# Kernel tuning notes

Measured on AMD Instinct MI355X. Metric: run time of the kernel, lower is better.

## Reference

```python
import jax, jax.numpy as jnp
import numpy as np

N = 4096      # batch (e.g. nodes)
MUL = 128     # multiplicity of every irrep chunk
INV_SQRT3 = 1.0 / float(np.sqrt(3.0))  # CG norm for 1x1->0 and 0x1->1 / 1x0->1
INV_SQRT6 = 1.0 / float(np.sqrt(6.0))  # CG norm for 1x1->1 (Levi-Civita / sqrt(6))

# Levi-Civita tensor eps[i,j,k]
_EPS = np.zeros((3, 3, 3), dtype=np.float32)
for a, b, c in [(0, 1, 2), (1, 2, 0), (2, 0, 1)]:
    _EPS[a, b, c] = 1.0
    _EPS[a, c, b] = -1.0
EPS = jnp.asarray(_EPS)


def setup_inputs() -> dict:
    key = jax.random.key(0)
    ks = jax.random.split(key, 9)
    # e3nn path normalization folded into weight init std:
    # std = 1/sqrt(mul1*mul2*num_paths_into_that_output_irrep)
    std2 = 1.0 / float(np.sqrt(MUL * MUL * 2))  # scalar out: 2 paths
    std3 = 1.0 / float(np.sqrt(MUL * MUL * 3))  # vector out: 3 paths
    W = (MUL, MUL, MUL)
    return {
        "x1_s": jax.random.normal(ks[0], (N, MUL), dtype=jnp.float32),
        "x1_v": jax.random.normal(ks[1], (N, MUL, 3), dtype=jnp.float32),
        "x2_s": jax.random.normal(ks[2], (N, MUL), dtype=jnp.float32),
        "x2_v": jax.random.normal(ks[3], (N, MUL, 3), dtype=jnp.float32),
        "w_sss": jax.random.normal(ks[4], W, dtype=jnp.float32) * std2,
        "w_vvs": jax.random.normal(ks[5], W, dtype=jnp.float32) * std2,
        "w_svv": jax.random.normal(ks[6], W, dtype=jnp.float32) * std3,
        "w_vsv": jax.random.normal(ks[7], W, dtype=jnp.float32) * std3,
        "w_vvv": jax.random.normal(ks[8], W, dtype=jnp.float32) * std3,
    }


def reference(x1_s, x1_v, x2_s, x2_v, w_sss, w_vvs, w_svv, w_vsv, w_vvv):
    # ---- paths into 0e (scalar) output ----
    # 0e x 0e -> 0e : CG = 1
    a = jnp.einsum('nu,uvw->nvw', x1_s, w_sss)           # [N,MUL,MUL]
    out_s = jnp.einsum('nvw,nv->nw', a, x2_s)            # [N,MUL]
    # 1o x 1o -> 0e : CG = delta_ij / sqrt(3)
    dot = jnp.einsum('nui,nvi->nuv', x1_v, x2_v) * INV_SQRT3
    out_s = out_s + jnp.einsum('nuv,uvw->nw', dot, w_vvs)
    # ---- paths into 1o (vector) output ----
    # 0e x 1o -> 1o : CG = delta / sqrt(3)
    b = jnp.einsum('nu,uvw->nvw', x1_s, w_svv)
    out_v = jnp.einsum('nvw,nvk->nwk', b, x2_v) * INV_SQRT3   # [N,MUL,3]
    # 1o x 0e -> 1o : CG = delta / sqrt(3)
    c = jnp.einsum('nv,uvw->nuw', x2_s, w_vsv)
    out_v = out_v + jnp.einsum('nuw,nuk->nwk', c, x1_v) * INV_SQRT3
    # 1o x 1o -> 1o : CG = eps_ijk / sqrt(6)  (cross product)
    c1 = jnp.einsum('nvj,ijk->nvik', x2_v, EPS)               # [N,MUL,3,3]
    cross = jnp.einsum('nui,nvik->nuvk', x1_v, c1)            # [N,MUL,MUL,3]
    out_v = out_v + jnp.einsum('nuvk,uvw->nwk', cross, w_vvv) * INV_SQRT6
    # pack IrrepsArray 128x0e+128x1o as flat [N, 128 + 384]
    return jnp.concatenate([out_s, out_v.reshape(out_v.shape[0], -1)], axis=-1)
```

## Files before the change

kernel.cpp:

```cpp
#include <hip/hip_runtime.h>
#include <hip/hip_bf16.h>


typedef _Float16 f16;
typedef _Float16 f16x8 __attribute__((ext_vector_type(8)));
typedef _Float16 h2 __attribute__((ext_vector_type(2)));
typedef float f32x4 __attribute__((ext_vector_type(4)));
typedef unsigned u32;

#define WT_BYTES  (5u*4u*128u*4096u*2u)
#define X1_BYTES  (64u*4u*8192u*2u)
#define SLICE_EL  1310720u
#define CHUNK_EL  10240u

__device__ __forceinline__ h2 bc(u32 x){ union{u32 u; h2 h;} c; c.u=x; return c.h; }

union F8 { h2 h[4]; f16x8 v; };

__device__ __forceinline__ void gl_lds16(const f16* g, f16* l) {
    __builtin_amdgcn_global_load_lds(
        (const __attribute__((address_space(1))) void*)g,
        (__attribute__((address_space(3))) void*)l,
        16, 0, 0);
}

__global__ __launch_bounds__(256) void pack_w_kernel(
    const float* __restrict__ w0, const float* __restrict__ w1,
    const float* __restrict__ w2, const float* __restrict__ w3,
    const float* __restrict__ w4, f16* __restrict__ wt)
{
    __shared__ float tl[64][130];
    const int b = blockIdx.x;
    const int p = b >> 7;
    const int u = b & 127;
    const int usec = u >> 5;
    const int uin  = u & 31;
    const float* src = (p==0)?w0:(p==1)?w1:(p==2)?w2:(p==3)?w3:w4;
    const float scale = (p==0)?1.0f:(p==4)?0.40824829046386302f:0.57735026918962576f;

    for (int h = 0; h < 2; ++h) {
        const float* spR = src + (size_t)u*16384 + (size_t)h*8192;
        #pragma unroll
        for (int k = 0; k < 8; ++k) {
            const int e4 = (k*256 + threadIdx.x) * 4;
            const float4 v4 = *(const float4*)(spR + e4);
            const int vi = e4 >> 7, w = e4 & 127;
            tl[vi][w+0]=v4.x; tl[vi][w+1]=v4.y; tl[vi][w+2]=v4.z; tl[vi][w+3]=v4.w;
        }
        __syncthreads();
        #pragma unroll
        for (int k = 0; k < 4; ++k) {
            const int cid = k*256 + threadIdx.x;
            const int q     = cid & 3;
            const int wg    = (cid >> 2) & 127;
            const int vbh   = cid >> 9;
            const int vb    = h*2 + vbh;
            const int c     = vb*32 + uin;
            const int whalf = wg >> 6;
            const int wl    = wg & 63;
            const int qs    = q ^ ((wl >> 1) & 3);
            f16x8 t8;
            #pragma unroll
            for (int j = 0; j < 8; ++j)
                t8[j] = (f16)(tl[vbh*32 + q*8 + j][wg] * scale);
            *(f16x8*)(wt + (size_t)(usec*2 + whalf)*SLICE_EL + (size_t)c*CHUNK_EL
                          + p*2048 + wl*32 + qs*8) = t8;
        }
        __syncthreads();
    }
}

__global__ __launch_bounds__(256) void pack_x_kernel(
    const float* __restrict__ x1s, const float* __restrict__ x1v,
    const float* __restrict__ x2s, const float* __restrict__ x2v,
    f16* __restrict__ x1g, f16* __restrict__ x2g)
{
    if (blockIdx.x < 128) {
        __shared__ uint2 tl[128][33];
        const int nb = blockIdx.x;
        #pragma unroll
        for (int k = 0; k < 16; ++k) {
            const int idx = k*256 + threadIdx.x;
            const int u = idx & 127, nd = idx >> 7;
            const size_t i = (size_t)(nb*32 + nd)*128 + u;
            union { f16 h[4]; uint2 u2; } tp;
            tp.h[0] = (f16)x1s[i];
            tp.h[1] = (f16)x1v[i*3 + 0];
            tp.h[2] = (f16)x1v[i*3 + 1];
            tp.h[3] = (f16)x1v[i*3 + 2];
            tl[u][nd] = tp.u2;
        }
        __syncthreads();
        uint2* og = (uint2*)x1g;
        const int t = nb >> 1, nd0 = (nb & 1) * 32;
        #pragma unroll
        for (int k = 0; k < 16; ++k) {
            const int idx = k*256 + threadIdx.x;
            const int u = idx >> 5, nd = idx & 31;
            og[(((t*4 + (u>>5))*32 + (u&31)) << 6) + nd0 + nd] = tl[u][nd];
        }
    } else {
        const int tt = (blockIdx.x - 128)*256 + threadIdx.x;
        const int n = tt >> 7, v = tt & 127;
        const size_t b = (size_t)n*512;
        const size_t i = (size_t)n*128 + v;
        x2g[b +   0 + v] = (f16)x2s[i];
        x2g[b + 128 + v] = (f16)x2v[i*3 + 0];
        x2g[b + 256 + v] = (f16)x2v[i*3 + 1];
        x2g[b + 384 + v] = (f16)x2v[i*3 + 2];
    }
}

__global__ __launch_bounds__(256, 2) void tp_main(
    const f16* __restrict__ wt, const f16* __restrict__ x1g,
    const f16* __restrict__ x2g, float* __restrict__ out)
{
    __shared__ __align__(16) f16 wlds[3*CHUNK_EL];
    __shared__ __align__(16) f16 x1lds[8192];

    const int tid  = threadIdx.x;
    const int lane = tid & 63;
    const int wv   = tid >> 6;
    const int kg   = lane >> 4;
    const int lr   = lane & 15;

    const int b     = blockIdx.x;
    const int slice = b & 7;
    const int t     = b >> 3;
    const int usec  = slice >> 1;
    const int whalf = slice & 1;

    const f16* wstream = wt + (size_t)slice * SLICE_EL;

    int boff[4];
    #pragma unroll
    for (int ct = 0; ct < 4; ++ct) {
        const int wp = ct*16 + lr;
        boff[ct] = wp*32 + ((kg ^ ((wp >> 1) & 3)) * 8);
    }

    {
        const f16* src = x1g + ((size_t)(t*4 + usec) << 13);
        #pragma unroll
        for (int r = 0; r < 4; ++r)
            gl_lds16(src + r*2048 + wv*512 + lane*8, x1lds + r*2048 + wv*512 + lane*8);
    }
    #pragma unroll
    for (int k = 0; k < 2; ++k)
        #pragma unroll
        for (int r = 0; r < 5; ++r)
            gl_lds16(wstream + k*CHUNK_EL + r*2048 + tid*8,
                     wlds    + k*CHUNK_EL + r*2048 + tid*8);
    __syncthreads();

    f32x4 acc[4][4];
    #pragma unroll
    for (int c2 = 0; c2 < 4; ++c2)
        #pragma unroll
        for (int d = 0; d < 4; ++d)
            acc[c2][d] = (f32x4){0.f, 0.f, 0.f, 0.f};

    h2 xq[4][4];
    const f16* wsrc = wstream + 2*CHUNK_EL + tid*8;
    const f16* x2base = x2g + ((size_t)(t*64 + wv*16 + lr) << 9) + kg*8;
    const int nodel4 = (wv*16 + lr) * 4;

    auto body = [&](int c, int bi) __attribute__((always_inline)) {
        if ((c & 31) == 0) {
            const f16* xb = x2base + (c >> 5)*32;
            const uint4 h0 = *(const uint4*)(xb);
            const uint4 h1 = *(const uint4*)(xb + 128);
            const uint4 h2v = *(const uint4*)(xb + 256);
            const uint4 h3 = *(const uint4*)(xb + 384);
            xq[0][0]=bc(h0.x); xq[0][1]=bc(h0.y); xq[0][2]=bc(h0.z); xq[0][3]=bc(h0.w);
            xq[1][0]=bc(h1.x); xq[1][1]=bc(h1.y); xq[1][2]=bc(h1.z); xq[1][3]=bc(h1.w);
            xq[2][0]=bc(h2v.x); xq[2][1]=bc(h2v.y); xq[2][2]=bc(h2v.z); xq[2][3]=bc(h2v.w);
            xq[3][0]=bc(h3.x); xq[3][1]=bc(h3.y); xq[3][2]=bc(h3.z); xq[3][3]=bc(h3.w);
        }

        if (c < 127) { asm volatile("s_waitcnt vmcnt(5)" ::: "memory"); }
        else         { asm volatile("s_waitcnt vmcnt(0)" ::: "memory"); }
        __builtin_amdgcn_s_barrier();
        __builtin_amdgcn_sched_barrier(0);

        if (c < 126) {
            f16* dc = wlds + ((bi + 2) % 3)*CHUNK_EL + tid*8;
            #pragma unroll
            for (int r = 0; r < 5; ++r)
                gl_lds16(wsrc + r*2048, dc + r*2048);
        }
        wsrc += CHUNK_EL;

        const int u2 = c & 31;

        const uint2 h1 = *(const uint2*)(x1lds + u2*256 + nodel4);
        const h2 ps1 = bc(__builtin_amdgcn_perm(h1.x, h1.x, 0x01000100u));
        h2 pv[3];
        pv[0] = bc(__builtin_amdgcn_perm(h1.x, h1.x, 0x03020302u));
        pv[1] = bc(__builtin_amdgcn_perm(h1.y, h1.y, 0x01000100u));
        pv[2] = bc(__builtin_amdgcn_perm(h1.y, h1.y, 0x03020302u));

        F8 f0, f1, fa[3], fb[3], fc[3];
        #pragma unroll
        for (int j = 0; j < 4; ++j) {
            f0.h[j] = ps1 * xq[0][j];
            h2 d = pv[0] * xq[1][j];
            d = __builtin_elementwise_fma(pv[1], xq[2][j], d);
            f1.h[j] = __builtin_elementwise_fma(pv[2], xq[3][j], d);
        }
        #pragma unroll
        for (int k = 0; k < 3; ++k) {
            const int k1 = (k+1) % 3, k2 = (k+2) % 3;
            #pragma unroll
            for (int j = 0; j < 4; ++j) {
                fa[k].h[j] = ps1   * xq[1+k][j];
                fb[k].h[j] = pv[k] * xq[0][j];
                h2 tx = pv[k1] * xq[1+k2][j];
                fc[k].h[j] = __builtin_elementwise_fma(-pv[k2], xq[1+k1][j], tx);
            }
        }

        const f16* wb = wlds + bi*CHUNK_EL;
        __builtin_amdgcn_s_setprio(1);
        #pragma unroll
        for (int ct = 0; ct < 4; ++ct) {
            const f16x8 b0 = *(const f16x8*)(wb +    0 + boff[ct]);
            const f16x8 b1 = *(const f16x8*)(wb + 2048 + boff[ct]);
            const f16x8 b2 = *(const f16x8*)(wb + 4096 + boff[ct]);
            const f16x8 b3 = *(const f16x8*)(wb + 6144 + boff[ct]);
            const f16x8 b4 = *(const f16x8*)(wb + 8192 + boff[ct]);
            acc[ct][0] = __builtin_amdgcn_mfma_f32_16x16x32_f16(f0.v, b0, acc[ct][0], 0,0,0);
            acc[ct][0] = __builtin_amdgcn_mfma_f32_16x16x32_f16(f1.v, b1, acc[ct][0], 0,0,0);
            #pragma unroll
            for (int k = 0; k < 3; ++k) {
                acc[ct][1+k] = __builtin_amdgcn_mfma_f32_16x16x32_f16(fa[k].v, b2, acc[ct][1+k], 0,0,0);
                acc[ct][1+k] = __builtin_amdgcn_mfma_f32_16x16x32_f16(fb[k].v, b3, acc[ct][1+k], 0,0,0);
                acc[ct][1+k] = __builtin_amdgcn_mfma_f32_16x16x32_f16(fc[k].v, b4, acc[ct][1+k], 0,0,0);
            }
        }
        __builtin_amdgcn_s_setprio(0);
    };

    for (int cb = 0; cb < 126; cb += 3) {
        body(cb + 0, 0);
        body(cb + 1, 1);
        body(cb + 2, 2);
    }
    body(126, 0);
    body(127, 1);

    #pragma unroll
    for (int ct = 0; ct < 4; ++ct) {
        const int w = whalf*64 + ct*16 + lr;
        #pragma unroll
        for (int j = 0; j < 4; ++j) {
            const int n = t*64 + wv*16 + kg*4 + j;
            float* op = out + (size_t)n*512;
            unsafeAtomicAdd(op + w,             acc[ct][0][j]);
            unsafeAtomicAdd(op + 128 + w*3 + 0, acc[ct][1][j]);
            unsafeAtomicAdd(op + 128 + w*3 + 1, acc[ct][2][j]);
            unsafeAtomicAdd(op + 128 + w*3 + 2, acc[ct][3][j]);
        }
    }
}

extern "C" void kernel_launch(void* const* d_in, const int* in_sizes, int n_in,
                              void* d_out, int out_size, void* d_ws, size_t ws_size,
                              hipStream_t stream)
{
    const float* x1s = (const float*)d_in[0];
    const float* x1v = (const float*)d_in[1];
    const float* x2s = (const float*)d_in[2];
    const float* x2v = (const float*)d_in[3];
    const float* w0  = (const float*)d_in[4];
    const float* w1  = (const float*)d_in[5];
    const float* w2  = (const float*)d_in[6];
    const float* w3  = (const float*)d_in[7];
    const float* w4  = (const float*)d_in[8];

    f16* wtb = (f16*)d_ws;
    f16* x1g = (f16*)((char*)d_ws + WT_BYTES);
    f16* x2g = (f16*)((char*)d_ws + WT_BYTES + X1_BYTES);
    float* out = (float*)d_out;

    pack_w_kernel<<<640, 256, 0, stream>>>(w0, w1, w2, w3, w4, wtb);
    pack_x_kernel<<<2176, 256, 0, stream>>>(x1s, x1v, x2s, x2v, x1g, x2g);
    hipMemsetAsync(d_out, 0, (size_t)out_size*sizeof(float), stream);
    tp_main<<<512, 256, 0, stream>>>(wtb, x1g, x2g, out);
}
```

Baseline: 240.2 us.

## Split v-range into halves for 1024 blocks, double-buffer weights, drop x1 LDS staging

Splits each block's reduction over v into two halves, so 16 slices per node tile and twice as many blocks. The weight packing is relaid to match. LDS shrinks from triple to double buffering and x1 is read straight from global with a one-step prefetch instead of staged in LDS, so occupancy can rise to 4 blocks per CU. The cost is twice as many atomic adds on the output, a full vmcnt(0) wait each step where the old code kept loads in flight, and the removal of setprio.

```diff
diff --git a/kernel.cpp b/kernel.cpp
--- a/kernel.cpp
+++ b/kernel.cpp
@@ -10,7 +10,7 @@
 
 #define WT_BYTES  (5u*4u*128u*4096u*2u)
 #define X1_BYTES  (64u*4u*8192u*2u)
-#define SLICE_EL  1310720u
+#define SLICE_EL  655360u
 #define CHUNK_EL  10240u
 
 __device__ __forceinline__ h2 bc(u32 x){ union{u32 u; h2 h;} c; c.u=x; return c.h; }
@@ -55,15 +55,17 @@
             const int wg    = (cid >> 2) & 127;
             const int vbh   = cid >> 9;
             const int vb    = h*2 + vbh;
-            const int c     = vb*32 + uin;
+            const int vhalf = vb >> 1;
+            const int c     = (vb & 1)*32 + uin;
             const int whalf = wg >> 6;
             const int wl    = wg & 63;
             const int qs    = q ^ ((wl >> 1) & 3);
+            const int s     = usec*4 + whalf*2 + vhalf;
             f16x8 t8;
             #pragma unroll
             for (int j = 0; j < 8; ++j)
                 t8[j] = (f16)(tl[vbh*32 + q*8 + j][wg] * scale);
-            *(f16x8*)(wt + (size_t)(usec*2 + whalf)*SLICE_EL + (size_t)c*CHUNK_EL
+            *(f16x8*)(wt + (size_t)s*SLICE_EL + (size_t)c*CHUNK_EL
                           + p*2048 + wl*32 + qs*8) = t8;
         }
         __syncthreads();
@@ -111,12 +113,11 @@
     }
 }
 
-__global__ __launch_bounds__(256, 2) void tp_main(
+__global__ __launch_bounds__(256, 4) void tp_main(
     const f16* __restrict__ wt, const f16* __restrict__ x1g,
     const f16* __restrict__ x2g, float* __restrict__ out)
 {
-    __shared__ __align__(16) f16 wlds[3*CHUNK_EL];
-    __shared__ __align__(16) f16 x1lds[8192];
+    __shared__ __align__(16) f16 wlds[2*CHUNK_EL];
 
     const int tid  = threadIdx.x;
     const int lane = tid & 63;
@@ -125,12 +126,13 @@
     const int lr   = lane & 15;
 
     const int b     = blockIdx.x;
-    const int slice = b & 7;
-    const int t     = b >> 3;
-    const int usec  = slice >> 1;
-    const int whalf = slice & 1;
-
-    const f16* wstream = wt + (size_t)slice * SLICE_EL;
+    const int s     = b & 15;
+    const int t     = b >> 4;
+    const int usec  = s >> 2;
+    const int whalf = (s >> 1) & 1;
+    const int vhalf = s & 1;
+
+    const f16* wstream = wt + (size_t)s * SLICE_EL;
 
     int boff[4];
     #pragma unroll
@@ -139,18 +141,14 @@
         boff[ct] = wp*32 + ((kg ^ ((wp >> 1) & 3)) * 8);
     }
 
-    {
-        const f16* src = x1g + ((size_t)(t*4 + usec) << 13);
-        #pragma unroll
-        for (int r = 0; r < 4; ++r)
-            gl_lds16(src + r*2048 + wv*512 + lane*8, x1lds + r*2048 + wv*512 + lane*8);
-    }
-    #pragma unroll
-    for (int k = 0; k < 2; ++k)
-        #pragma unroll
-        for (int r = 0; r < 5; ++r)
-            gl_lds16(wstream + k*CHUNK_EL + r*2048 + tid*8,
-                     wlds    + k*CHUNK_EL + r*2048 + tid*8);
+    const int nodel4 = (wv*16 + lr) * 4;
+    const f16* x1base = x1g + (size_t)(t*4 + usec) * 8192 + nodel4;
+    const f16* x2base = x2g + ((size_t)(t*64 + wv*16 + lr) << 9) + kg*8;
+
+    #pragma unroll
+    for (int r = 0; r < 5; ++r)
+        gl_lds16(wstream + r*2048 + tid*8, wlds + r*2048 + tid*8);
+    uint2 h1c = *(const uint2*)(x1base);
     __syncthreads();
 
     f32x4 acc[4][4];
@@ -161,13 +159,73 @@
             acc[c2][d] = (f32x4){0.f, 0.f, 0.f, 0.f};
 
     h2 xq[4][4];
-    const f16* wsrc = wstream + 2*CHUNK_EL + tid*8;
-    const f16* x2base = x2g + ((size_t)(t*64 + wv*16 + lr) << 9) + kg*8;
-    const int nodel4 = (wv*16 + lr) * 4;
-
-    auto body = [&](int c, int bi) __attribute__((always_inline)) {
-        if ((c & 31) == 0) {
-            const f16* xb = x2base + (c >> 5)*32;
+    const f16* wsrc = wstream + CHUNK_EL + tid*8;
+
+    auto body = [&](int cc, int buf) __attribute__((always_inline)) {
+        asm volatile("s_waitcnt vmcnt(0)" ::: "memory");
+        __builtin_amdgcn_s_barrier();
+        __builtin_amdgcn_sched_barrier(0);
+
+        if (cc < 63) {
+            f16* dc = wlds + (buf^1)*CHUNK_EL + tid*8;
+            #pragma unroll
+            for (int r = 0; r < 5; ++r)
+                gl_lds16(wsrc + r*2048, dc + r*2048);
+        }
+        wsrc += CHUNK_EL;
+
+        const uint2 h1n = *(const uint2*)(x1base + (((cc + 1) & 31) << 8));
+
+        const h2 ps1 = bc(__builtin_amdgcn_perm(h1c.x, h1c.x, 0x01000100u));
+        h2 pv[3];
+        pv[0] = bc(__builtin_amdgcn_perm(h1c.x, h1c.x, 0x03020302u));
+        pv[1] = bc(__builtin_amdgcn_perm(h1c.y, h1c.y, 0x01000100u));
+        pv[2] = bc(__builtin_amdgcn_perm(h1c.y, h1c.y, 0x03020302u));
+
+        F8 f0, f1, fa[3], fb[3], fc[3];
+        #pragma unroll
+        for (int j = 0; j < 4; ++j) {
+            f0.h[j] = ps1 * xq[0][j];
+            h2 d = pv[0] * xq[1][j];
+            d = __builtin_elementwise_fma(pv[1], xq[2][j], d);
+            f1.h[j] = __builtin_elementwise_fma(pv[2], xq[3][j], d);
+        }
+        #pragma unroll
+        for (int k = 0; k < 3; ++k) {
+            const int k1 = (k+1) % 3, k2 = (k+2) % 3;
+            #pragma unroll
+            for (int j = 0; j < 4; ++j) {
+                fa[k].h[j] = ps1   * xq[1+k][j];
+                fb[k].h[j] = pv[k] * xq[0][j];
+                h2 tx = pv[k1] * xq[1+k2][j];
+                fc[k].h[j] = __builtin_elementwise_fma(-pv[k2], xq[1+k1][j], tx);
+            }
+        }
+
+        const f16* wb = wlds + buf*CHUNK_EL;
+        #pragma unroll
+        for (int ct = 0; ct < 4; ++ct) {
+            const f16x8 b0 = *(const f16x8*)(wb +    0 + boff[ct]);
+            const f16x8 b1 = *(const f16x8*)(wb + 2048 + boff[ct]);
+            const f16x8 b2 = *(const f16x8*)(wb + 4096 + boff[ct]);
+            const f16x8 b3 = *(const f16x8*)(wb + 6144 + boff[ct]);
+            const f16x8 b4 = *(const f16x8*)(wb + 8192 + boff[ct]);
+            acc[ct][0] = __builtin_amdgcn_mfma_f32_16x16x32_f16(f0.v, b0, acc[ct][0], 0,0,0);
+            acc[ct][0] = __builtin_amdgcn_mfma_f32_16x16x32_f16(f1.v, b1, acc[ct][0], 0,0,0);
+            #pragma unroll
+            for (int k = 0; k < 3; ++k) {
+                acc[ct][1+k] = __builtin_amdgcn_mfma_f32_16x16x32_f16(fa[k].v, b2, acc[ct][1+k], 0,0,0);
+                acc[ct][1+k] = __builtin_amdgcn_mfma_f32_16x16x32_f16(fb[k].v, b3, acc[ct][1+k], 0,0,0);
+                acc[ct][1+k] = __builtin_amdgcn_mfma_f32_16x16x32_f16(fc[k].v, b4, acc[ct][1+k], 0,0,0);
+            }
+        }
+        h1c = h1n;
+    };
+
+    for (int vbl = 0; vbl < 2; ++vbl) {
+        const int vb = vhalf*2 + vbl;
+        {
+            const f16* xb = x2base + vb*32;
             const uint4 h0 = *(const uint4*)(xb);
             const uint4 h1 = *(const uint4*)(xb + 128);
             const uint4 h2v = *(const uint4*)(xb + 256);
@@ -177,77 +235,11 @@
             xq[2][0]=bc(h2v.x); xq[2][1]=bc(h2v.y); xq[2][2]=bc(h2v.z); xq[2][3]=bc(h2v.w);
             xq[3][0]=bc(h3.x); xq[3][1]=bc(h3.y); xq[3][2]=bc(h3.z); xq[3][3]=bc(h3.w);
         }
-
-        if (c < 127) { asm volatile("s_waitcnt vmcnt(5)" ::: "memory"); }
-        else         { asm volatile("s_waitcnt vmcnt(0)" ::: "memory"); }
-        __builtin_amdgcn_s_barrier();
-        __builtin_amdgcn_sched_barrier(0);
-
-        if (c < 126) {
-            f16* dc = wlds + ((bi + 2) % 3)*CHUNK_EL + tid*8;
-            #pragma unroll
-            for (int r = 0; r < 5; ++r)
-                gl_lds16(wsrc + r*2048, dc + r*2048);
-        }
-        wsrc += CHUNK_EL;
-
-        const int u2 = c & 31;
-
-        const uint2 h1 = *(const uint2*)(x1lds + u2*256 + nodel4);
-        const h2 ps1 = bc(__builtin_amdgcn_perm(h1.x, h1.x, 0x01000100u));
-        h2 pv[3];
-        pv[0] = bc(__builtin_amdgcn_perm(h1.x, h1.x, 0x03020302u));
-        pv[1] = bc(__builtin_amdgcn_perm(h1.y, h1.y, 0x01000100u));
-        pv[2] = bc(__builtin_amdgcn_perm(h1.y, h1.y, 0x03020302u));
-
-        F8 f0, f1, fa[3], fb[3], fc[3];
-        #pragma unroll
-        for (int j = 0; j < 4; ++j) {
-            f0.h[j] = ps1 * xq[0][j];
-            h2 d = pv[0] * xq[1][j];
-            d = __builtin_elementwise_fma(pv[1], xq[2][j], d);
-            f1.h[j] = __builtin_elementwise_fma(pv[2], xq[3][j], d);
-        }
-        #pragma unroll
-        for (int k = 0; k < 3; ++k) {
-            const int k1 = (k+1) % 3, k2 = (k+2) % 3;
-            #pragma unroll
-            for (int j = 0; j < 4; ++j) {
-                fa[k].h[j] = ps1   * xq[1+k][j];
-                fb[k].h[j] = pv[k] * xq[0][j];
-                h2 tx = pv[k1] * xq[1+k2][j];
-                fc[k].h[j] = __builtin_elementwise_fma(-pv[k2], xq[1+k1][j], tx);
-            }
-        }
-
-        const f16* wb = wlds + bi*CHUNK_EL;
-        __builtin_amdgcn_s_setprio(1);
-        #pragma unroll
-        for (int ct = 0; ct < 4; ++ct) {
-            const f16x8 b0 = *(const f16x8*)(wb +    0 + boff[ct]);
-            const f16x8 b1 = *(const f16x8*)(wb + 2048 + boff[ct]);
-            const f16x8 b2 = *(const f16x8*)(wb + 4096 + boff[ct]);
-            const f16x8 b3 = *(const f16x8*)(wb + 6144 + boff[ct]);
-            const f16x8 b4 = *(const f16x8*)(wb + 8192 + boff[ct]);
-            acc[ct][0] = __builtin_amdgcn_mfma_f32_16x16x32_f16(f0.v, b0, acc[ct][0], 0,0,0);
-            acc[ct][0] = __builtin_amdgcn_mfma_f32_16x16x32_f16(f1.v, b1, acc[ct][0], 0,0,0);
-            #pragma unroll
-            for (int k = 0; k < 3; ++k) {
-                acc[ct][1+k] = __builtin_amdgcn_mfma_f32_16x16x32_f16(fa[k].v, b2, acc[ct][1+k], 0,0,0);
-                acc[ct][1+k] = __builtin_amdgcn_mfma_f32_16x16x32_f16(fb[k].v, b3, acc[ct][1+k], 0,0,0);
-                acc[ct][1+k] = __builtin_amdgcn_mfma_f32_16x16x32_f16(fc[k].v, b4, acc[ct][1+k], 0,0,0);
-            }
-        }
-        __builtin_amdgcn_s_setprio(0);
-    };
-
-    for (int cb = 0; cb < 126; cb += 3) {
-        body(cb + 0, 0);
-        body(cb + 1, 1);
-        body(cb + 2, 2);
-    }
-    body(126, 0);
-    body(127, 1);
+        for (int u2b = 0; u2b < 32; u2b += 2) {
+            body(vbl*32 + u2b + 0, 0);
+            body(vbl*32 + u2b + 1, 1);
+        }
+    }
 
     #pragma unroll
     for (int ct = 0; ct < 4; ++ct) {
@@ -286,5 +278,5 @@
     pack_w_kernel<<<640, 256, 0, stream>>>(w0, w1, w2, w3, w4, wtb);
     pack_x_kernel<<<2176, 256, 0, stream>>>(x1s, x1v, x2s, x2v, x1g, x2g);
     hipMemsetAsync(d_out, 0, (size_t)out_size*sizeof(float), stream);
-    tp_main<<<512, 256, 0, stream>>>(wtb, x1g, x2g, out);
-}
+    tp_main<<<1024, 256, 0, stream>>>(wtb, x1g, x2g, out);
+}
```

Measured after the change: 368.1 us. +53.2%, slower.

## Split each chunk into four phases interleaving LDS reads, async staging, and MFMAs

Applied to the files above, without the earlier changes.

Restructures the per-chunk body into four phases, one per output column tile. Each phase issues its LDS B-fragment reads and part of the next chunk's global-to-LDS staging, then a barrier and lgkmcnt wait, then its MFMAs. The aim is to spread the staging loads and LDS traffic across the MFMA work instead of bunching them at the start. In exchange it adds two extra workgroup barriers per phase, about eight more per chunk, which may serialize the waves.

```diff
diff --git a/kernel.cpp b/kernel.cpp
--- a/kernel.cpp
+++ b/kernel.cpp
@@ -169,11 +169,11 @@
         if ((c & 31) == 0) {
             const f16* xb = x2base + (c >> 5)*32;
             const uint4 h0 = *(const uint4*)(xb);
-            const uint4 h1 = *(const uint4*)(xb + 128);
+            const uint4 h1x = *(const uint4*)(xb + 128);
             const uint4 h2v = *(const uint4*)(xb + 256);
             const uint4 h3 = *(const uint4*)(xb + 384);
             xq[0][0]=bc(h0.x); xq[0][1]=bc(h0.y); xq[0][2]=bc(h0.z); xq[0][3]=bc(h0.w);
-            xq[1][0]=bc(h1.x); xq[1][1]=bc(h1.y); xq[1][2]=bc(h1.z); xq[1][3]=bc(h1.w);
+            xq[1][0]=bc(h1x.x); xq[1][1]=bc(h1x.y); xq[1][2]=bc(h1x.z); xq[1][3]=bc(h1x.w);
             xq[2][0]=bc(h2v.x); xq[2][1]=bc(h2v.y); xq[2][2]=bc(h2v.z); xq[2][3]=bc(h2v.w);
             xq[3][0]=bc(h3.x); xq[3][1]=bc(h3.y); xq[3][2]=bc(h3.z); xq[3][3]=bc(h3.w);
         }
@@ -183,62 +183,76 @@
         __builtin_amdgcn_s_barrier();
         __builtin_amdgcn_sched_barrier(0);
 
-        if (c < 126) {
-            f16* dc = wlds + ((bi + 2) % 3)*CHUNK_EL + tid*8;
-            #pragma unroll
-            for (int r = 0; r < 5; ++r)
-                gl_lds16(wsrc + r*2048, dc + r*2048);
-        }
-        wsrc += CHUNK_EL;
-
         const int u2 = c & 31;
-
-        const uint2 h1 = *(const uint2*)(x1lds + u2*256 + nodel4);
-        const h2 ps1 = bc(__builtin_amdgcn_perm(h1.x, h1.x, 0x01000100u));
-        h2 pv[3];
-        pv[0] = bc(__builtin_amdgcn_perm(h1.x, h1.x, 0x03020302u));
-        pv[1] = bc(__builtin_amdgcn_perm(h1.y, h1.y, 0x01000100u));
-        pv[2] = bc(__builtin_amdgcn_perm(h1.y, h1.y, 0x03020302u));
+        const f16* wb = wlds + bi*CHUNK_EL;
+        f16* dst = wlds + ((bi + 2) % 3)*CHUNK_EL + tid*8;
+        const bool do_stage = (c < 126);
 
         F8 f0, f1, fa[3], fb[3], fc[3];
-        #pragma unroll
-        for (int j = 0; j < 4; ++j) {
-            f0.h[j] = ps1 * xq[0][j];
-            h2 d = pv[0] * xq[1][j];
-            d = __builtin_elementwise_fma(pv[1], xq[2][j], d);
-            f1.h[j] = __builtin_elementwise_fma(pv[2], xq[3][j], d);
-        }
-        #pragma unroll
-        for (int k = 0; k < 3; ++k) {
-            const int k1 = (k+1) % 3, k2 = (k+2) % 3;
-            #pragma unroll
-            for (int j = 0; j < 4; ++j) {
-                fa[k].h[j] = ps1   * xq[1+k][j];
-                fb[k].h[j] = pv[k] * xq[0][j];
-                h2 tx = pv[k1] * xq[1+k2][j];
-                fc[k].h[j] = __builtin_elementwise_fma(-pv[k2], xq[1+k1][j], tx);
+
+        #pragma unroll
+        for (int ph = 0; ph < 4; ++ph) {
+            uint2 h1;
+            if (ph == 0) h1 = *(const uint2*)(x1lds + u2*256 + nodel4);
+            const f16* fbp = wb + boff[ph];
+            const f16x8 B0 = *(const f16x8*)(fbp +    0);
+            const f16x8 B1 = *(const f16x8*)(fbp + 2048);
+            const f16x8 B2 = *(const f16x8*)(fbp + 4096);
+            const f16x8 B3 = *(const f16x8*)(fbp + 6144);
+            const f16x8 B4 = *(const f16x8*)(fbp + 8192);
+
+            if (do_stage) {
+                if (ph == 0) {
+                    gl_lds16(wsrc +    0, dst +    0);
+                    gl_lds16(wsrc + 2048, dst + 2048);
+                } else {
+                    gl_lds16(wsrc + (ph+1)*2048, dst + (ph+1)*2048);
+                }
             }
-        }
-
-        const f16* wb = wlds + bi*CHUNK_EL;
-        __builtin_amdgcn_s_setprio(1);
-        #pragma unroll
-        for (int ct = 0; ct < 4; ++ct) {
-            const f16x8 b0 = *(const f16x8*)(wb +    0 + boff[ct]);
-            const f16x8 b1 = *(const f16x8*)(wb + 2048 + boff[ct]);
-            const f16x8 b2 = *(const f16x8*)(wb + 4096 + boff[ct]);
-            const f16x8 b3 = *(const f16x8*)(wb + 6144 + boff[ct]);
-            const f16x8 b4 = *(const f16x8*)(wb + 8192 + boff[ct]);
-            acc[ct][0] = __builtin_amdgcn_mfma_f32_16x16x32_f16(f0.v, b0, acc[ct][0], 0,0,0);
-            acc[ct][0] = __builtin_amdgcn_mfma_f32_16x16x32_f16(f1.v, b1, acc[ct][0], 0,0,0);
+
+            __builtin_amdgcn_s_barrier();
+            asm volatile("s_waitcnt lgkmcnt(0)" ::: "memory");
+            __builtin_amdgcn_sched_barrier(0);
+
+            if (ph == 0) {
+                const h2 ps1 = bc(__builtin_amdgcn_perm(h1.x, h1.x, 0x01000100u));
+                h2 pv[3];
+                pv[0] = bc(__builtin_amdgcn_perm(h1.x, h1.x, 0x03020302u));
+                pv[1] = bc(__builtin_amdgcn_perm(h1.y, h1.y, 0x01000100u));
+                pv[2] = bc(__builtin_amdgcn_perm(h1.y, h1.y, 0x03020302u));
+                #pragma unroll
+                for (int j = 0; j < 4; ++j) {
+                    f0.h[j] = ps1 * xq[0][j];
+                    h2 d = pv[0] * xq[1][j];
+                    d = __builtin_elementwise_fma(pv[1], xq[2][j], d);
+                    f1.h[j] = __builtin_elementwise_fma(pv[2], xq[3][j], d);
+                }
+                #pragma unroll
+                for (int k = 0; k < 3; ++k) {
+                    const int k1 = (k+1) % 3, k2 = (k+2) % 3;
+                    #pragma unroll
+                    for (int j = 0; j < 4; ++j) {
+                        fa[k].h[j] = ps1   * xq[1+k][j];
+                        fb[k].h[j] = pv[k] * xq[0][j];
+                        h2 tx = pv[k1] * xq[1+k2][j];
+                        fc[k].h[j] = __builtin_elementwise_fma(-pv[k2], xq[1+k1][j], tx);
+                    }
+                }
+            }
+
+            __builtin_amdgcn_s_setprio(1);
+            acc[ph][0] = __builtin_amdgcn_mfma_f32_16x16x32_f16(f0.v, B0, acc[ph][0], 0,0,0);
+            acc[ph][0] = __builtin_amdgcn_mfma_f32_16x16x32_f16(f1.v, B1, acc[ph][0], 0,0,0);
             #pragma unroll
             for (int k = 0; k < 3; ++k) {
-                acc[ct][1+k] = __builtin_amdgcn_mfma_f32_16x16x32_f16(fa[k].v, b2, acc[ct][1+k], 0,0,0);
-                acc[ct][1+k] = __builtin_amdgcn_mfma_f32_16x16x32_f16(fb[k].v, b3, acc[ct][1+k], 0,0,0);
-                acc[ct][1+k] = __builtin_amdgcn_mfma_f32_16x16x32_f16(fc[k].v, b4, acc[ct][1+k], 0,0,0);
+                acc[ph][1+k] = __builtin_amdgcn_mfma_f32_16x16x32_f16(fa[k].v, B2, acc[ph][1+k], 0,0,0);
+                acc[ph][1+k] = __builtin_amdgcn_mfma_f32_16x16x32_f16(fb[k].v, B3, acc[ph][1+k], 0,0,0);
+                acc[ph][1+k] = __builtin_amdgcn_mfma_f32_16x16x32_f16(fc[k].v, B4, acc[ph][1+k], 0,0,0);
             }
-        }
-        __builtin_amdgcn_s_setprio(0);
+            __builtin_amdgcn_s_setprio(0);
+            __builtin_amdgcn_s_barrier();
+        }
+        wsrc += CHUNK_EL;
     };
 
     for (int cb = 0; cb < 126; cb += 3) {
```

Measured after the change: 251.2 us. 1.05x slower.
